# Performance work log

Hardware: AMD Instinct MI355X
Metric: run time of the kernel (lower is better)

The kernel has to match this reference:

```python
import jax, jax.numpy as jnp
import numpy as np

NUM_HEADS = 16
ROPE_BASE = 10000.0
MAX_POS = 4096


def _rope_tables(head_dim):
    inv_freq = 1.0 / (ROPE_BASE ** (np.arange(0, head_dim, 2, dtype=np.float32) / head_dim))
    freqs = np.arange(MAX_POS, dtype=np.float32)[:, None] * inv_freq[None, :]
    emb = np.concatenate([freqs, freqs], axis=-1)  # [MAX_POS, head_dim]
    return jnp.asarray(np.cos(emb)), jnp.asarray(np.sin(emb))


def _rotate_half(x):
    d = x.shape[-1] // 2
    return jnp.concatenate([-x[..., d:], x[..., :d]], axis=-1)


def _apply_rope(x, pos, cos_t, sin_t):
    # x: [B,H,S,D], pos: [B,S]
    cos = cos_t[pos][:, None]  # [B,1,S,D]
    sin = sin_t[pos][:, None]
    return x * cos + _rotate_half(x) * sin


def setup_inputs() -> dict:
    key = jax.random.key(0)
    ks = jax.random.split(key, 8)
    B, N, M, C = 2, 2048, 2048, 1024
    s = 1.0 / np.sqrt(C)
    return {
        "query": jax.random.normal(ks[0], (B, N, C), jnp.float32),
        "key": jax.random.normal(ks[1], (B, M, C), jnp.float32),
        "query_pos": jnp.broadcast_to(jnp.arange(N, dtype=jnp.int32), (B, N)),
        "key_pos": jnp.broadcast_to(jnp.arange(M, dtype=jnp.int32), (B, M)),
        "Wq": jax.random.normal(ks[2], (C, C), jnp.float32) * s,
        "bq": jnp.zeros((C,), jnp.float32),
        "Wk": jax.random.normal(ks[3], (C, C), jnp.float32) * s,
        "Wv": jax.random.normal(ks[4], (C, C), jnp.float32) * s,
        "bv": jnp.zeros((C,), jnp.float32),
        "Wo": jax.random.normal(ks[5], (C, C), jnp.float32) * s,
        "bo": jnp.zeros((C,), jnp.float32),
    }


def reference(query, key, query_pos, key_pos, Wq, bq, Wk, Wv, bv, Wo, bo):
    B, N, C = query.shape
    M = key.shape[1]
    H = NUM_HEADS
    D = C // H
    scale = D ** -0.5
    cos_t, sin_t = _rope_tables(D)

    value = key  # value defaults to key
    identity = query

    q = (query @ Wq.T + bq).reshape(B, N, H, D).transpose(0, 2, 1, 3)
    k = (key @ Wk.T).reshape(B, M, H, D).transpose(0, 2, 1, 3)
    v = (value @ Wv.T + bv).reshape(B, M, H, D).transpose(0, 2, 1, 3)

    q = _apply_rope(q, query_pos, cos_t, sin_t)
    k = _apply_rope(k, key_pos, cos_t, sin_t)

    attn = jnp.einsum('bhnd,bhmd->bhnm', q, k) * scale
    attn = jax.nn.softmax(attn, axis=-1)
    x = jnp.einsum('bhnm,bhmd->bhnd', attn, v)  # [B,H,N,D]
    x = x.transpose(0, 2, 1, 3).reshape(B, N, C)
    x = x @ Wo.T + bo
    return x + identity
```

## Files before the change

### kernel.cpp

```cpp
#include <hip/hip_runtime.h>
#include <hip/hip_bf16.h>
#include <stdint.h>

#define B_ 2
#define N_ 2048
#define M_ 2048
#define C_ 1024
#define H_ 16
#define D_ 64

typedef __attribute__((ext_vector_type(8))) short s16x8;
typedef __attribute__((ext_vector_type(4))) short s16x4;
typedef __attribute__((ext_vector_type(4))) float f32x4;
typedef __attribute__((ext_vector_type(16))) float f32x16;

__device__ __attribute__((always_inline)) inline short f2b(float f){
    __hip_bfloat16 h = __float2bfloat16(f); short s; __builtin_memcpy(&s, &h, 2); return s;
}
__device__ __attribute__((always_inline)) inline float b2f(short s){
    __hip_bfloat16 h; __builtin_memcpy(&h, &s, 2); return __bfloat162float(h);
}

#define MFMA16(a,b,c) __builtin_amdgcn_mfma_f32_16x16x32_bf16(a,b,c,0,0,0)
#define MFMA32(a,b,c) __builtin_amdgcn_mfma_f32_32x32x16_bf16(a,b,c,0,0,0)

__device__ __attribute__((always_inline)) inline void gl_lds16(const void* g, void* l){
    __builtin_amdgcn_global_load_lds((__attribute__((address_space(1))) void*)g,
                                     (__attribute__((address_space(3))) void*)l, 16, 0, 0);
}
__device__ __attribute__((always_inline)) inline unsigned cvtpk(float lo, float hi){
    unsigned r;
    asm("v_cvt_pk_bf16_f32 %0, %1, %2" : "=v"(r) : "v"(lo), "v"(hi));
    return r;
}
__device__ __attribute__((always_inline)) inline void lane32swap(unsigned &a, unsigned &b){
    asm("v_permlane32_swap_b32 %0, %1" : "+v"(a), "+v"(b));
}

__global__ void cvt_all(const float* __restrict__ q, const float* __restrict__ k,
                        const float* __restrict__ wq, const float* __restrict__ wk,
                        const float* __restrict__ wv, const float* __restrict__ wo,
                        short* __restrict__ dst){
    long i = ((long)blockIdx.x * 256 + threadIdx.x) * 8;
    const float* src; long off;
    if      (i <  4194304L){ src = q;  off = i; }
    else if (i <  8388608L){ src = k;  off = i - 4194304L; }
    else if (i <  9437184L){ src = wq; off = i - 8388608L; }
    else if (i < 10485760L){ src = wk; off = i - 9437184L; }
    else if (i < 11534336L){ src = wv; off = i - 10485760L; }
    else                   { src = wo; off = i - 11534336L; }
    float4 a = *(const float4*)(src + off);
    float4 b = *(const float4*)(src + off + 4);
    s16x8 o;
    o[0]=f2b(a.x); o[1]=f2b(a.y); o[2]=f2b(a.z); o[3]=f2b(a.w);
    o[4]=f2b(b.x); o[5]=f2b(b.y); o[6]=f2b(b.z); o[7]=f2b(b.w);
    *(s16x8*)(dst + i) = o;
}

__global__ __launch_bounds__(256, 3) void gemm_qkv(
    const short* __restrict__ qbf, const short* __restrict__ kbf,
    const short* __restrict__ W,
    const float* __restrict__ bq, const float* __restrict__ bv,
    const int* __restrict__ kpos,
    short* __restrict__ qproj, short* __restrict__ kproj, short* __restrict__ vT)
{
    __shared__ short sb[8704];
    short* As = sb;
    short* Bs = sb + 4096;
    const int n0 = blockIdx.x * 128, m0 = blockIdx.y * 128;
    const int sel = n0 >> 10;
    const short* A = (sel == 0) ? qbf : kbf;
    const int tid = threadIdx.x, lane = tid & 63, wave = tid >> 6;
    const int quad = lane >> 4, l16 = lane & 15;
    const int wr = (wave >> 1) * 64, wc = (wave & 1) * 64;
    const int srow = lane >> 2, scol = (lane & 3) * 8;

    f32x4 acc[4][4] = {};

    const short* Ag = A + (size_t)(m0 + wave * 32 + srow) * C_ + scol;
    const short* Bg = W + (size_t)(n0 + wave * 32 + srow) * C_ + scol;
    short* lA0 = As + (wave * 32) * 32;
    short* lA1 = As + (wave * 32 + 16) * 32;
    short* lB0 = Bs + (wave * 32) * 32;
    short* lB1 = Bs + (wave * 32 + 16) * 32;

    for (int k0 = 0; k0 < C_; k0 += 32){
        __syncthreads();
        gl_lds16(Ag + k0, lA0);
        gl_lds16(Ag + k0 + 16 * (size_t)C_, lA1);
        gl_lds16(Bg + k0, lB0);
        gl_lds16(Bg + k0 + 16 * (size_t)C_, lB1);
        __syncthreads();
        s16x8 af[4], bfr[4];
        #pragma unroll
        for (int t = 0; t < 4; t++) af[t]  = *(const s16x8*)&As[(wr + t*16 + l16) * 32 + quad * 8];
        #pragma unroll
        for (int t = 0; t < 4; t++) bfr[t] = *(const s16x8*)&Bs[(wc + t*16 + l16) * 32 + quad * 8];
        #pragma unroll
        for (int i = 0; i < 4; i++)
            #pragma unroll
            for (int j = 0; j < 4; j++)
                acc[i][j] = MFMA16(af[i], bfr[j], acc[i][j]);
    }

    if (sel == 0){
        #pragma unroll
        for (int j = 0; j < 4; j++){
            int c = n0 + wc + j * 16 + l16;
            float bb = bq[c];
            #pragma unroll
            for (int i = 0; i < 4; i++){
                int row = m0 + wr + i * 16 + quad * 4;
                #pragma unroll
                for (int r = 0; r < 4; r++)
                    qproj[(size_t)(row + r) * C_ + c] = f2b(acc[i][j][r] + bb);
            }
        }
    } else if (sel == 1){
        #pragma unroll
        for (int j2 = 0; j2 < 2; j2++){
            int c1 = n0 - 1024 + wc + j2 * 16 + l16;
            int irot = c1 & 63;
            float invf = exp2f((float)irot * (-13.287712379549449f / 32.0f));
            #pragma unroll
            for (int i = 0; i < 4; i++){
                int row = m0 + wr + i * 16 + quad * 4;
                #pragma unroll
                for (int r = 0; r < 4; r++){
                    float pos = (float)kpos[row + r];
                    float ang = pos * invf;
                    float cs = __cosf(ang), sn = __sinf(ang);
                    float x1 = acc[i][j2][r], x2 = acc[i][j2 + 2][r];
                    kproj[(size_t)(row + r) * C_ + c1]      = f2b(x1 * cs - x2 * sn);
                    kproj[(size_t)(row + r) * C_ + c1 + 32] = f2b(x2 * cs + x1 * sn);
                }
            }
        }
    } else {
        short* Vt = sb;
        const int bat = m0 >> 11;
        const int mbase = m0 & 2047;
        #pragma unroll
        for (int p = 0; p < 2; p++){
            __syncthreads();
            if ((wave & 1) == p){
                #pragma unroll
                for (int j = 0; j < 4; j++){
                    int c_local = j * 16 + l16;
                    float bb = bv[n0 - 2048 + p * 64 + c_local];
                    #pragma unroll
                    for (int i = 0; i < 4; i++){
                        int row = wr + i * 16 + quad * 4;
                        unsigned u0 = (unsigned)(unsigned short)f2b(acc[i][j][0] + bb) |
                                      ((unsigned)(unsigned short)f2b(acc[i][j][1] + bb) << 16);
                        unsigned u1 = (unsigned)(unsigned short)f2b(acc[i][j][2] + bb) |
                                      ((unsigned)(unsigned short)f2b(acc[i][j][3] + bb) << 16);
                        uint2 u; u.x = u0; u.y = u1;
                        *(uint2*)&Vt[c_local * 136 + row] = u;
                    }
                }
            }
            __syncthreads();
            #pragma unroll
            for (int it = 0; it < 4; it++){
                int qq = it * 256 + tid;
                int c_local = qq >> 4, mm = (qq & 15) * 8;
                int colg = n0 - 2048 + p * 64 + c_local;
                int hh = colg >> 6, dd = colg & 63;
                s16x8 v = *(const s16x8*)&Vt[c_local * 136 + mm];
                *(s16x8*)&vT[(((size_t)(bat * H_ + hh)) * D_ + dd) * M_ + mbase + mm] = v;
            }
        }
    }
}

__global__ __launch_bounds__(256, 4) void gemm_out(
    const short* __restrict__ A, const short* __restrict__ W,
    const float* __restrict__ bias, const float* __restrict__ resid,
    float* __restrict__ outf)
{
    __shared__ short As[128 * 32];
    __shared__ short Bs[64 * 32];
    const int n0 = blockIdx.x * 64, m0 = blockIdx.y * 128;
    const int tid = threadIdx.x, lane = tid & 63, wave = tid >> 6;
    const int quad = lane >> 4, l16 = lane & 15;
    const int srow = lane >> 2, scol = (lane & 3) * 8;

    f32x4 acc[2][4] = {};
    const short* Ag = A + (size_t)(m0 + wave * 32 + srow) * C_ + scol;
    const short* Bg = W + (size_t)(n0 + wave * 16 + srow) * C_ + scol;
    short* lA0 = As + (wave * 32) * 32;
    short* lA1 = As + (wave * 32 + 16) * 32;
    short* lB  = Bs + (wave * 16) * 32;

    for (int k0 = 0; k0 < C_; k0 += 32){
        __syncthreads();
        gl_lds16(Ag + k0, lA0);
        gl_lds16(Ag + k0 + 16 * (size_t)C_, lA1);
        gl_lds16(Bg + k0, lB);
        __syncthreads();
        s16x8 af[2], bfr[4];
        #pragma unroll
        for (int t = 0; t < 2; t++) af[t]  = *(const s16x8*)&As[(wave*32 + t*16 + l16) * 32 + quad * 8];
        #pragma unroll
        for (int t = 0; t < 4; t++) bfr[t] = *(const s16x8*)&Bs[(t*16 + l16) * 32 + quad * 8];
        #pragma unroll
        for (int i = 0; i < 2; i++)
            #pragma unroll
            for (int j = 0; j < 4; j++)
                acc[i][j] = MFMA16(af[i], bfr[j], acc[i][j]);
    }

    #pragma unroll
    for (int j = 0; j < 4; j++){
        int c = n0 + j * 16 + l16;
        float bb = bias[c];
        #pragma unroll
        for (int i = 0; i < 2; i++){
            int row = m0 + wave * 32 + i * 16 + quad * 4;
            #pragma unroll
            for (int r = 0; r < 4; r++){
                size_t idx = (size_t)(row + r) * C_ + c;
                outf[idx] = acc[i][j][r] + bb + resid[idx];
            }
        }
    }
}

__global__ __launch_bounds__(256, 2) void flash_attn(
    const short* __restrict__ q, const short* __restrict__ k,
    const short* __restrict__ vt, short* __restrict__ o,
    const int* __restrict__ qpos)
{
    __shared__ short smem[35328];
    const int b = blockIdx.y >> 4, h = blockIdx.y & 15;
    const int n0 = blockIdx.x * 128;
    const int tid = threadIdx.x, lane = tid & 63, wave = tid >> 6;
    const int hi = lane >> 5, l32 = lane & 31;
    const int wq = wave & 1, kq = wave >> 1;

    s16x8 qf[2][4];
    const float fac = 0.18033688011112042f;
    #pragma unroll
    for (int qt = 0; qt < 2; qt++){
        int qrow = n0 + wq * 64 + qt * 32 + l32;
        const short* qg = &q[((size_t)(b * N_ + qrow)) * C_ + h * D_];
        float pos = (float)qpos[b * N_ + qrow];
        s16x8 raw[4];
        #pragma unroll
        for (int c = 0; c < 4; c++) raw[c] = *(const s16x8*)&qg[c * 16 + hi * 8];
        #pragma unroll
        for (int c = 0; c < 2; c++){
            s16x8 olo, ohi8;
            #pragma unroll
            for (int j = 0; j < 8; j++){
                int irot = c * 16 + hi * 8 + j;
                float invf = exp2f((float)irot * (-13.287712379549449f / 32.0f));
                float ang = pos * invf;
                float cs = __cosf(ang), sn = __sinf(ang);
                float x1 = b2f(raw[c][j]), x2 = b2f(raw[c + 2][j]);
                olo[j]  = f2b((x1 * cs - x2 * sn) * fac);
                ohi8[j] = f2b((x2 * cs + x1 * sn) * fac);
            }
            qf[qt][c] = olo; qf[qt][c + 2] = ohi8;
        }
    }

    const short* kg = k  + (size_t)(b * M_) * C_ + h * D_;
    const short* vg = vt + ((size_t)(b * H_ + h)) * D_ * M_;
    const int srow0 = tid >> 3, sseg = (tid & 7) * 8;

    union V8 { s16x8 v; uint2 u[2]; };
    V8 kreg[2], vreg[2];

    #pragma unroll
    for (int ii = 0; ii < 2; ii++){
        int row = srow0 + 32 * ii;
        kreg[ii].v = *(const s16x8*)&kg[(size_t)row * C_ + sseg];
        vreg[ii].v = *(const s16x8*)&vg[(size_t)row * M_ + sseg];
    }
    #pragma unroll
    for (int ii = 0; ii < 2; ii++){
        int row = srow0 + 32 * ii;
        short* kd = &smem[row * 68 + sseg];
        *(uint2*)kd = kreg[ii].u[0]; *(uint2*)(kd + 4) = kreg[ii].u[1];
        short* vd = &smem[17408 + row * 68 + sseg];
        *(uint2*)vd = vreg[ii].u[0]; *(uint2*)(vd + 4) = vreg[ii].u[1];
    }
    #pragma unroll
    for (int ii = 0; ii < 2; ii++){
        int row = srow0 + 32 * ii;
        kreg[ii].v = *(const s16x8*)&kg[(size_t)(64 + row) * C_ + sseg];
        vreg[ii].v = *(const s16x8*)&vg[(size_t)row * M_ + 64 + sseg];
    }
    asm volatile("s_waitcnt lgkmcnt(0)" ::: "memory");
    __builtin_amdgcn_s_barrier();

    f32x16 zero16 = {};
    f32x16 oacc[2][2] = {zero16, zero16, zero16, zero16};
    float lacc[2] = {0.f, 0.f};

    for (int st = 0; st < 32; st++){
        const int bi = st & 3;
        const short* Kp = &smem[bi * 4352];
        const short* Vp = &smem[17408 + bi * 4352];

        s16x4 kf[4][2];
        #pragma unroll
        for (int c = 0; c < 4; c++){
            const short* a = &Kp[(kq * 32 + l32) * 68 + c * 16 + hi * 8];
            kf[c][0] = *(const s16x4*)a; kf[c][1] = *(const s16x4*)(a + 4);
        }
        s16x8 vf[2][2];
        #pragma unroll
        for (int dt = 0; dt < 2; dt++)
            #pragma unroll
            for (int c = 0; c < 2; c++){
                const short* a = &Vp[(dt * 32 + l32) * 68 + kq * 32 + c * 16 + hi * 8];
                vf[dt][c] = __builtin_shufflevector(*(const s16x4*)a, *(const s16x4*)(a + 4),
                                                    0,1,2,3,4,5,6,7);
            }

        s16x8 pf[2][2];
        #pragma unroll
        for (int qt = 0; qt < 2; qt++){
            f32x16 sv = {};
            #pragma unroll
            for (int c = 0; c < 4; c++){
                s16x8 ka = __builtin_shufflevector(kf[c][0], kf[c][1], 0,1,2,3,4,5,6,7);
                sv = MFMA32(ka, qf[qt][c], sv);
            }
            float pe[16];
            #pragma unroll
            for (int e = 0; e < 16; e++) pe[e] = __builtin_amdgcn_exp2f(sv[e]);
            float ls = 0.f;
            #pragma unroll
            for (int e = 0; e < 16; e += 4) ls += (pe[e] + pe[e+1]) + (pe[e+2] + pe[e+3]);
            lacc[qt] += ls;
            #pragma unroll
            for (int c = 0; c < 2; c++){
                unsigned a1 = cvtpk(pe[8*c + 0], pe[8*c + 1]);
                unsigned a2 = cvtpk(pe[8*c + 2], pe[8*c + 3]);
                unsigned b1 = cvtpk(pe[8*c + 4], pe[8*c + 5]);
                unsigned b2 = cvtpk(pe[8*c + 6], pe[8*c + 7]);
                lane32swap(a1, b1);
                lane32swap(a2, b2);
                union { unsigned u[4]; s16x8 v; } pk;
                pk.u[0] = a1; pk.u[1] = a2; pk.u[2] = b1; pk.u[3] = b2;
                pf[qt][c] = pk.v;
            }
        }

        #pragma unroll
        for (int qt = 0; qt < 2; qt++)
            #pragma unroll
            for (int dt = 0; dt < 2; dt++)
                #pragma unroll
                for (int c = 0; c < 2; c++)
                    oacc[qt][dt] = MFMA32(pf[qt][c], vf[dt][c], oacc[qt][dt]);

        if (st < 31){
            int bn = (st + 1) & 3;
            #pragma unroll
            for (int ii = 0; ii < 2; ii++){
                int row = srow0 + 32 * ii;
                short* kd = &smem[bn * 4352 + row * 68 + sseg];
                *(uint2*)kd = kreg[ii].u[0]; *(uint2*)(kd + 4) = kreg[ii].u[1];
                short* vd = &smem[17408 + bn * 4352 + row * 68 + sseg];
                *(uint2*)vd = vreg[ii].u[0]; *(uint2*)(vd + 4) = vreg[ii].u[1];
            }
        }
        if (st < 30){
            #pragma unroll
            for (int ii = 0; ii < 2; ii++){
                int row = srow0 + 32 * ii;
                kreg[ii].v = *(const s16x8*)&kg[((size_t)((st + 2) * 64 + row)) * C_ + sseg];
                vreg[ii].v = *(const s16x8*)&vg[(size_t)row * M_ + (st + 2) * 64 + sseg];
            }
        }
        asm volatile("s_waitcnt lgkmcnt(0)" ::: "memory");
        __builtin_amdgcn_s_barrier();
    }

    __syncthreads();

    float* LO   = (float*)smem;
    float* Lsum = (float*)&smem[34816];
    float* Linv = Lsum + 128;

    float l0[2];
    #pragma unroll
    for (int qt = 0; qt < 2; qt++)
        l0[qt] = lacc[qt] + __shfl_xor(lacc[qt], 32);

    if (kq == 1){
        #pragma unroll
        for (int qt = 0; qt < 2; qt++)
            Lsum[wq * 64 + qt * 32 + l32] = l0[qt];
        #pragma unroll
        for (int qt = 0; qt < 2; qt++)
            #pragma unroll
            for (int dt = 0; dt < 2; dt++)
                #pragma unroll
                for (int e = 0; e < 16; e++){
                    int qrow = wq * 64 + qt * 32 + (e & 3) + 8 * (e >> 2) + 4 * hi;
                    LO[qrow * 65 + dt * 32 + l32] = oacc[qt][dt][e];
                }
    }
    __syncthreads();
    if (kq == 0){
        #pragma unroll
        for (int qt = 0; qt < 2; qt++){
            float lt = l0[qt] + Lsum[wq * 64 + qt * 32 + l32];
            Linv[wq * 64 + qt * 32 + l32] = 1.0f / lt;
        }
        asm volatile("s_waitcnt lgkmcnt(0)" ::: "memory");
        #pragma unroll
        for (int qt = 0; qt < 2; qt++)
            #pragma unroll
            for (int dt = 0; dt < 2; dt++)
                #pragma unroll
                for (int e = 0; e < 16; e++){
                    int qrow = wq * 64 + qt * 32 + (e & 3) + 8 * (e >> 2) + 4 * hi;
                    float val = (oacc[qt][dt][e] + LO[qrow * 65 + dt * 32 + l32]) * Linv[qrow];
                    o[((size_t)(b * N_ + n0 + qrow)) * C_ + h * D_ + dt * 32 + l32] = f2b(val);
                }
    }
}

extern "C" void kernel_launch(void* const* d_in, const int* in_sizes, int n_in,
                              void* d_out, int out_size, void* d_ws, size_t ws_size,
                              hipStream_t stream) {
    const float* query = (const float*)d_in[0];
    const float* key   = (const float*)d_in[1];
    const int*   qpos  = (const int*)d_in[2];
    const int*   kpos  = (const int*)d_in[3];
    const float* Wq    = (const float*)d_in[4];
    const float* bq    = (const float*)d_in[5];
    const float* Wk    = (const float*)d_in[6];
    const float* Wv    = (const float*)d_in[7];
    const float* bv    = (const float*)d_in[8];
    const float* Wo    = (const float*)d_in[9];
    const float* bo    = (const float*)d_in[10];
    float* out = (float*)d_out;

    const size_t E4M = (size_t)4 * 1024 * 1024;
    const size_t E1M = (size_t)1024 * 1024;
    short* ws    = (short*)d_ws;
    short* qbf   = ws;
    short* kbf   = qbf   + E4M;
    short* wqkvb = kbf   + E4M;
    short* wob   = wqkvb + 3 * E1M;
    short* qproj = wob   + E1M;
    short* kproj = qproj + E4M;
    short* vT    = kproj + E4M;
    short* attn  = qbf;

    cvt_all<<<6144, 256, 0, stream>>>(query, key, Wq, Wk, Wv, Wo, ws);

    gemm_qkv<<<dim3(24, 32), 256, 0, stream>>>(qbf, kbf, wqkvb, bq, bv, kpos,
                                               qproj, kproj, vT);

    flash_attn<<<dim3(16, 32), 256, 0, stream>>>(qproj, kproj, vT, attn, qpos);

    gemm_out<<<dim3(16, 32), 256, 0, stream>>>(attn, wob, bo, query, out);
}
```

Before: 205.8 us.

## Software-pipeline attention loop so QK MFMA of next tile overlaps softmax/PV

Splits the attention inner loop into QK-score, softmax+PV finish, and staging phases, then software-pipelines them with double-buffered score and V-fragment registers. The QK matmul for tile st+1 is issued before the exp/pack/PV of tile st, so matrix instructions can overlap the transcendental and pack work. It raises register pressure (two sets of scores and V fragments live at once), which may reduce occupancy or cause spills.

```diff
diff --git a/kernel.cpp b/kernel.cpp
--- a/kernel.cpp
+++ b/kernel.cpp
@@ -300,18 +300,19 @@
     f32x16 oacc[2][2] = {zero16, zero16, zero16, zero16};
     float lacc[2] = {0.f, 0.f};
 
-    for (int st = 0; st < 32; st++){
+    f32x16 svA[2], svB[2];
+    s16x8 vfA[2][2], vfB[2][2];
+
+    auto QKSTEP = [&](int st, f32x16 (&sv)[2], s16x8 (&vf)[2][2]){
         const int bi = st & 3;
         const short* Kp = &smem[bi * 4352];
         const short* Vp = &smem[17408 + bi * 4352];
-
         s16x4 kf[4][2];
         #pragma unroll
         for (int c = 0; c < 4; c++){
             const short* a = &Kp[(kq * 32 + l32) * 68 + c * 16 + hi * 8];
             kf[c][0] = *(const s16x4*)a; kf[c][1] = *(const s16x4*)(a + 4);
         }
-        s16x8 vf[2][2];
         #pragma unroll
         for (int dt = 0; dt < 2; dt++)
             #pragma unroll
@@ -320,19 +321,25 @@
                 vf[dt][c] = __builtin_shufflevector(*(const s16x4*)a, *(const s16x4*)(a + 4),
                                                     0,1,2,3,4,5,6,7);
             }
-
-        s16x8 pf[2][2];
         #pragma unroll
         for (int qt = 0; qt < 2; qt++){
-            f32x16 sv = {};
+            f32x16 sv0 = {};
             #pragma unroll
             for (int c = 0; c < 4; c++){
                 s16x8 ka = __builtin_shufflevector(kf[c][0], kf[c][1], 0,1,2,3,4,5,6,7);
-                sv = MFMA32(ka, qf[qt][c], sv);
-            }
+                sv0 = MFMA32(ka, qf[qt][c], sv0);
+            }
+            sv[qt] = sv0;
+        }
+    };
+
+    auto FINISH = [&](const f32x16 (&sv)[2], const s16x8 (&vf)[2][2]){
+        s16x8 pf[2][2];
+        #pragma unroll
+        for (int qt = 0; qt < 2; qt++){
             float pe[16];
             #pragma unroll
-            for (int e = 0; e < 16; e++) pe[e] = __builtin_amdgcn_exp2f(sv[e]);
+            for (int e = 0; e < 16; e++) pe[e] = __builtin_amdgcn_exp2f(sv[qt][e]);
             float ls = 0.f;
             #pragma unroll
             for (int e = 0; e < 16; e += 4) ls += (pe[e] + pe[e+1]) + (pe[e+2] + pe[e+3]);
@@ -350,7 +357,6 @@
                 pf[qt][c] = pk.v;
             }
         }
-
         #pragma unroll
         for (int qt = 0; qt < 2; qt++)
             #pragma unroll
@@ -358,7 +364,9 @@
                 #pragma unroll
                 for (int c = 0; c < 2; c++)
                     oacc[qt][dt] = MFMA32(pf[qt][c], vf[dt][c], oacc[qt][dt]);
-
+    };
+
+    auto STAGE = [&](int st){
         if (st < 31){
             int bn = (st + 1) & 3;
             #pragma unroll
@@ -380,7 +388,21 @@
         }
         asm volatile("s_waitcnt lgkmcnt(0)" ::: "memory");
         __builtin_amdgcn_s_barrier();
-    }
+    };
+
+    QKSTEP(0, svA, vfA);
+    STAGE(0);
+    for (int stp = 1; stp < 31; stp += 2){
+        QKSTEP(stp, svB, vfB);
+        FINISH(svA, vfA);
+        STAGE(stp);
+        QKSTEP(stp + 1, svA, vfA);
+        FINISH(svB, vfB);
+        STAGE(stp + 1);
+    }
+    QKSTEP(31, svB, vfB);
+    FINISH(svA, vfA);
+    FINISH(svB, vfB);
 
     __syncthreads();
 
```

After: 219.8 us. 1.07x slower.

## Software-pipeline QK^T of the next KV tile with softmax/PV of current

Applied to the files above, without the earlier changes.

Restructures the attention main loop so the QK^T MFMAs for tile st are issued before the exp/pack/PV work of tile st-1, using two alternating score register sets (svA and svB) in a manually unrolled-by-two loop with a prologue and epilogue. The intent is to overlap the matrix-core work with the exp2 and conversion work on the vector units, hiding MFMA latency. The cost is 32 extra live floats per thread, which raises register pressure under the existing launch bounds and could cause spills or lower occupancy.

```diff
diff --git a/kernel.cpp b/kernel.cpp
--- a/kernel.cpp
+++ b/kernel.cpp
@@ -227,6 +227,95 @@
     }
 }
 
+#define QK_STEP(ST, SV) do {                                                          \
+    const short* Kp_ = &smem[((ST) & 3) * 4352];                                      \
+    s16x4 kfa_[4][2];                                                                 \
+    _Pragma("unroll")                                                                 \
+    for (int c = 0; c < 4; c++){                                                      \
+        const short* a_ = &Kp_[(kq * 32 + l32) * 68 + c * 16 + hi * 8];               \
+        kfa_[c][0] = *(const s16x4*)a_; kfa_[c][1] = *(const s16x4*)(a_ + 4);         \
+    }                                                                                 \
+    _Pragma("unroll")                                                                 \
+    for (int qt = 0; qt < 2; qt++){                                                   \
+        f32x16 sv0_ = {};                                                             \
+        _Pragma("unroll")                                                             \
+        for (int c = 0; c < 4; c++){                                                  \
+            s16x8 ka_ = __builtin_shufflevector(kfa_[c][0], kfa_[c][1],               \
+                                                0,1,2,3,4,5,6,7);                     \
+            sv0_ = MFMA32(ka_, qf[qt][c], sv0_);                                      \
+        }                                                                             \
+        SV[qt] = sv0_;                                                                \
+    }                                                                                 \
+} while(0)
+
+#define FINISH_STEP(ST, SV) do {                                                      \
+    const short* Vp_ = &smem[17408 + ((ST) & 3) * 4352];                              \
+    s16x8 vfa_[2][2];                                                                 \
+    _Pragma("unroll")                                                                 \
+    for (int dt = 0; dt < 2; dt++)                                                    \
+        _Pragma("unroll")                                                             \
+        for (int c = 0; c < 2; c++){                                                  \
+            const short* a_ = &Vp_[(dt * 32 + l32) * 68 + kq * 32 + c * 16 + hi * 8]; \
+            vfa_[dt][c] = __builtin_shufflevector(*(const s16x4*)a_,                  \
+                                                  *(const s16x4*)(a_ + 4),            \
+                                                  0,1,2,3,4,5,6,7);                   \
+        }                                                                             \
+    s16x8 pfa_[2][2];                                                                 \
+    _Pragma("unroll")                                                                 \
+    for (int qt = 0; qt < 2; qt++){                                                   \
+        _Pragma("unroll")                                                             \
+        for (int e = 0; e < 16; e++) SV[qt][e] = __builtin_amdgcn_exp2f(SV[qt][e]);   \
+        float ls_ = 0.f;                                                              \
+        _Pragma("unroll")                                                             \
+        for (int e = 0; e < 16; e += 4)                                               \
+            ls_ += (SV[qt][e] + SV[qt][e+1]) + (SV[qt][e+2] + SV[qt][e+3]);           \
+        lacc[qt] += ls_;                                                              \
+        _Pragma("unroll")                                                             \
+        for (int c = 0; c < 2; c++){                                                  \
+            unsigned a1_ = cvtpk(SV[qt][8*c + 0], SV[qt][8*c + 1]);                   \
+            unsigned a2_ = cvtpk(SV[qt][8*c + 2], SV[qt][8*c + 3]);                   \
+            unsigned b1_ = cvtpk(SV[qt][8*c + 4], SV[qt][8*c + 5]);                   \
+            unsigned b2_ = cvtpk(SV[qt][8*c + 6], SV[qt][8*c + 7]);                   \
+            lane32swap(a1_, b1_);                                                     \
+            lane32swap(a2_, b2_);                                                     \
+            union { unsigned u[4]; s16x8 v; } pk_;                                    \
+            pk_.u[0] = a1_; pk_.u[1] = a2_; pk_.u[2] = b1_; pk_.u[3] = b2_;           \
+            pfa_[qt][c] = pk_.v;                                                      \
+        }                                                                             \
+    }                                                                                 \
+    _Pragma("unroll")                                                                 \
+    for (int qt = 0; qt < 2; qt++)                                                    \
+        _Pragma("unroll")                                                             \
+        for (int dt = 0; dt < 2; dt++)                                                \
+            _Pragma("unroll")                                                         \
+            for (int c = 0; c < 2; c++)                                               \
+                oacc[qt][dt] = MFMA32(pfa_[qt][c], vfa_[dt][c], oacc[qt][dt]);        \
+} while(0)
+
+#define STAGE_STEP(ST) do {                                                           \
+    if ((ST) < 31){                                                                   \
+        int bn_ = ((ST) + 1) & 3;                                                     \
+        _Pragma("unroll")                                                             \
+        for (int ii = 0; ii < 2; ii++){                                               \
+            int row_ = srow0 + 32 * ii;                                               \
+            short* kd_ = &smem[bn_ * 4352 + row_ * 68 + sseg];                        \
+            *(uint2*)kd_ = kreg[ii].u[0]; *(uint2*)(kd_ + 4) = kreg[ii].u[1];         \
+            short* vd_ = &smem[17408 + bn_ * 4352 + row_ * 68 + sseg];                \
+            *(uint2*)vd_ = vreg[ii].u[0]; *(uint2*)(vd_ + 4) = vreg[ii].u[1];         \
+        }                                                                             \
+    }                                                                                 \
+    if ((ST) < 30){                                                                   \
+        _Pragma("unroll")                                                             \
+        for (int ii = 0; ii < 2; ii++){                                               \
+            int row_ = srow0 + 32 * ii;                                               \
+            kreg[ii].v = *(const s16x8*)&kg[((size_t)(((ST) + 2) * 64 + row_)) * C_ + sseg]; \
+            vreg[ii].v = *(const s16x8*)&vg[(size_t)row_ * M_ + ((ST) + 2) * 64 + sseg];     \
+        }                                                                             \
+    }                                                                                 \
+    asm volatile("s_waitcnt lgkmcnt(0)" ::: "memory");                                \
+    __builtin_amdgcn_s_barrier();                                                     \
+} while(0)
+
 __global__ __launch_bounds__(256, 2) void flash_attn(
     const short* __restrict__ q, const short* __restrict__ k,
     const short* __restrict__ vt, short* __restrict__ o,
@@ -300,87 +389,21 @@
     f32x16 oacc[2][2] = {zero16, zero16, zero16, zero16};
     float lacc[2] = {0.f, 0.f};
 
-    for (int st = 0; st < 32; st++){
-        const int bi = st & 3;
-        const short* Kp = &smem[bi * 4352];
-        const short* Vp = &smem[17408 + bi * 4352];
-
-        s16x4 kf[4][2];
-        #pragma unroll
-        for (int c = 0; c < 4; c++){
-            const short* a = &Kp[(kq * 32 + l32) * 68 + c * 16 + hi * 8];
-            kf[c][0] = *(const s16x4*)a; kf[c][1] = *(const s16x4*)(a + 4);
-        }
-        s16x8 vf[2][2];
-        #pragma unroll
-        for (int dt = 0; dt < 2; dt++)
-            #pragma unroll
-            for (int c = 0; c < 2; c++){
-                const short* a = &Vp[(dt * 32 + l32) * 68 + kq * 32 + c * 16 + hi * 8];
-                vf[dt][c] = __builtin_shufflevector(*(const s16x4*)a, *(const s16x4*)(a + 4),
-                                                    0,1,2,3,4,5,6,7);
-            }
-
-        s16x8 pf[2][2];
-        #pragma unroll
-        for (int qt = 0; qt < 2; qt++){
-            f32x16 sv = {};
-            #pragma unroll
-            for (int c = 0; c < 4; c++){
-                s16x8 ka = __builtin_shufflevector(kf[c][0], kf[c][1], 0,1,2,3,4,5,6,7);
-                sv = MFMA32(ka, qf[qt][c], sv);
-            }
-            float pe[16];
-            #pragma unroll
-            for (int e = 0; e < 16; e++) pe[e] = __builtin_amdgcn_exp2f(sv[e]);
-            float ls = 0.f;
-            #pragma unroll
-            for (int e = 0; e < 16; e += 4) ls += (pe[e] + pe[e+1]) + (pe[e+2] + pe[e+3]);
-            lacc[qt] += ls;
-            #pragma unroll
-            for (int c = 0; c < 2; c++){
-                unsigned a1 = cvtpk(pe[8*c + 0], pe[8*c + 1]);
-                unsigned a2 = cvtpk(pe[8*c + 2], pe[8*c + 3]);
-                unsigned b1 = cvtpk(pe[8*c + 4], pe[8*c + 5]);
-                unsigned b2 = cvtpk(pe[8*c + 6], pe[8*c + 7]);
-                lane32swap(a1, b1);
-                lane32swap(a2, b2);
-                union { unsigned u[4]; s16x8 v; } pk;
-                pk.u[0] = a1; pk.u[1] = a2; pk.u[2] = b1; pk.u[3] = b2;
-                pf[qt][c] = pk.v;
-            }
-        }
-
-        #pragma unroll
-        for (int qt = 0; qt < 2; qt++)
-            #pragma unroll
-            for (int dt = 0; dt < 2; dt++)
-                #pragma unroll
-                for (int c = 0; c < 2; c++)
-                    oacc[qt][dt] = MFMA32(pf[qt][c], vf[dt][c], oacc[qt][dt]);
-
-        if (st < 31){
-            int bn = (st + 1) & 3;
-            #pragma unroll
-            for (int ii = 0; ii < 2; ii++){
-                int row = srow0 + 32 * ii;
-                short* kd = &smem[bn * 4352 + row * 68 + sseg];
-                *(uint2*)kd = kreg[ii].u[0]; *(uint2*)(kd + 4) = kreg[ii].u[1];
-                short* vd = &smem[17408 + bn * 4352 + row * 68 + sseg];
-                *(uint2*)vd = vreg[ii].u[0]; *(uint2*)(vd + 4) = vreg[ii].u[1];
-            }
-        }
-        if (st < 30){
-            #pragma unroll
-            for (int ii = 0; ii < 2; ii++){
-                int row = srow0 + 32 * ii;
-                kreg[ii].v = *(const s16x8*)&kg[((size_t)((st + 2) * 64 + row)) * C_ + sseg];
-                vreg[ii].v = *(const s16x8*)&vg[(size_t)row * M_ + (st + 2) * 64 + sseg];
-            }
-        }
-        asm volatile("s_waitcnt lgkmcnt(0)" ::: "memory");
-        __builtin_amdgcn_s_barrier();
-    }
+    f32x16 svA[2], svB[2];
+
+    QK_STEP(0, svA);
+    STAGE_STEP(0);
+    for (int st = 1; st <= 29; st += 2){
+        QK_STEP(st, svB);
+        FINISH_STEP(st - 1, svA);
+        STAGE_STEP(st);
+        QK_STEP(st + 1, svA);
+        FINISH_STEP(st, svB);
+        STAGE_STEP(st + 1);
+    }
+    QK_STEP(31, svB);
+    FINISH_STEP(30, svA);
+    FINISH_STEP(31, svB);
 
     __syncthreads();
 
```

After: 211.7 us. 1.03x slower.
